# Optimization experiments

Measured on AMD Instinct MI355X. Metric: run time of the kernel, lower is better.

Reference implementation:

```python
import jax, jax.numpy as jnp
import numpy as np

POOL_H, POOL_W = 7, 7


def crop_and_resize(fmap, boxes, box_idx, ph, pw):
    """TF-style bilinear crop_and_resize. fmap [B,H,W,C], boxes [N,4] (y1,x1,y2,x2)
    normalized, box_idx [N] int32 -> [N,ph,pw,C]."""
    H, W = fmap.shape[1], fmap.shape[2]
    y1, x1, y2, x2 = boxes[:, 0], boxes[:, 1], boxes[:, 2], boxes[:, 3]
    gy = jnp.arange(ph, dtype=boxes.dtype) / (ph - 1)  # [ph]
    gx = jnp.arange(pw, dtype=boxes.dtype) / (pw - 1)  # [pw]
    in_y = (y1[:, None] + (y2 - y1)[:, None] * gy) * (H - 1)  # [N,ph]
    in_x = (x1[:, None] + (x2 - x1)[:, None] * gx) * (W - 1)  # [N,pw]
    y0f = jnp.floor(in_y)
    x0f = jnp.floor(in_x)
    wy = (in_y - y0f)[:, :, None, None]  # [N,ph,1,1]
    wx = (in_x - x0f)[:, None, :, None]  # [N,1,pw,1]
    y0 = jnp.clip(y0f.astype(jnp.int32), 0, H - 1)
    y1i = jnp.clip(y0 + 1, 0, H - 1)
    x0 = jnp.clip(x0f.astype(jnp.int32), 0, W - 1)
    x1i = jnp.clip(x0 + 1, 0, W - 1)
    b = box_idx[:, None, None]
    tl = fmap[b, y0[:, :, None], x0[:, None, :]]   # [N,ph,pw,C]
    tr = fmap[b, y0[:, :, None], x1i[:, None, :]]
    bl = fmap[b, y1i[:, :, None], x0[:, None, :]]
    br = fmap[b, y1i[:, :, None], x1i[:, None, :]]
    top = tl + (tr - tl) * wx
    bot = bl + (br - bl) * wx
    return top + (bot - top) * wy


def compute_roi_level(boxes, image_shape):
    # boxes [B,N,4] normalized (y1,x1,y2,x2)
    h = boxes[..., 2] - boxes[..., 0]
    w = boxes[..., 3] - boxes[..., 1]
    image_area = image_shape[0] * image_shape[1]
    lvl = jnp.log2(jnp.sqrt(h * w) / (224.0 / jnp.sqrt(image_area)))
    lvl = jnp.minimum(5.0, jnp.maximum(2.0, 4.0 + jnp.round(lvl)))
    return jax.lax.stop_gradient(lvl).astype(jnp.int32)  # [B,N]


def setup_inputs() -> dict:
    key = jax.random.key(0)
    kb, k2, k3, k4, k5 = jax.random.split(key, 5)
    B, N, C = 2, 1000, 256
    raw = jax.random.uniform(kb, (B, N, 2, 2), dtype=jnp.float32)
    lo = raw.min(axis=2)   # (y1, x1)
    hi = raw.max(axis=2)   # (y2, x2)
    boxes = jnp.concatenate([lo, hi], axis=-1)  # [B,N,4]
    image_shape = jnp.array([1024.0, 1024.0], dtype=jnp.float32)
    P2 = jax.random.normal(k2, (B, 256, 256, C), dtype=jnp.float32)
    P3 = jax.random.normal(k3, (B, 128, 128, C), dtype=jnp.float32)
    P4 = jax.random.normal(k4, (B, 64, 64, C), dtype=jnp.float32)
    P5 = jax.random.normal(k5, (B, 32, 32, C), dtype=jnp.float32)
    return {"boxes": boxes, "image_shape": image_shape,
            "P2": P2, "P3": P3, "P4": P4, "P5": P5}


def reference(boxes, image_shape, P2, P3, P4, P5):
    B, N = boxes.shape[0], boxes.shape[1]
    C = P2.shape[-1]
    levels = compute_roi_level(boxes, image_shape).reshape(-1)  # [B*N]
    flat_boxes = boxes.reshape(-1, 4)
    box_idx = jnp.repeat(jnp.arange(B, dtype=jnp.int32), N)
    pooled = jnp.zeros((B * N, POOL_H, POOL_W, C), dtype=P2.dtype)
    for lvl, fmap in zip((2, 3, 4, 5), (P2, P3, P4, P5)):
        crops = crop_and_resize(fmap, flat_boxes, box_idx, POOL_H, POOL_W)
        mask = (levels == lvl)[:, None, None, None]
        pooled = jnp.where(mask, crops, pooled)
    # The TF version partitions boxes per level then sorts back to original
    # (batch, box) order; the masked-select form yields the identical tensor.
    return pooled.reshape(B, N, POOL_H, POOL_W, C)
```

## Files before the change

### kernel.cpp

```cpp
#include <hip/hip_runtime.h>


#define POOL 7
#define CCH 256

__global__ __launch_bounds__(256) void roi_align_kernel(
    const float* __restrict__ boxes,
    const float* __restrict__ ish,
    const float* __restrict__ P2,
    const float* __restrict__ P3,
    const float* __restrict__ P4,
    const float* __restrict__ P5,
    float* __restrict__ out,
    int n_cells, int N)
{
    int cell = blockIdx.x * 4 + (threadIdx.x >> 6);
    if (cell >= n_cells) return;
    int lane = threadIdx.x & 63;

    int px  = cell % POOL;
    int t   = cell / POOL;
    int py  = t % POOL;
    int n   = t / POOL;
    int b   = n / N;

    float y1 = boxes[n * 4 + 0];
    float x1 = boxes[n * 4 + 1];
    float y2 = boxes[n * 4 + 2];
    float x2 = boxes[n * 4 + 3];
    float h = y2 - y1;
    float w = x2 - x1;

    float area = ish[0] * ish[1];
    float lvl  = log2f(sqrtf(h * w) / (224.0f / sqrtf(area)));
    float Lf   = fminf(5.0f, fmaxf(2.0f, 4.0f + rintf(lvl)));
    int   L    = (int)Lf;

    const float* fmap;
    int H;
    if (L == 2)      { fmap = P2; H = 256; }
    else if (L == 3) { fmap = P3; H = 128; }
    else if (L == 4) { fmap = P4; H = 64;  }
    else             { fmap = P5; H = 32;  }
    int W = H;

    float gy = (float)py / (float)(POOL - 1);
    float gx = (float)px / (float)(POOL - 1);
    float in_y = (y1 + h * gy) * (float)(H - 1);
    float in_x = (x1 + w * gx) * (float)(W - 1);
    float y0f = floorf(in_y);
    float x0f = floorf(in_x);
    float wy = in_y - y0f;
    float wx = in_x - x0f;
    int y0  = min(max((int)y0f, 0), H - 1);
    int y1i = min(y0 + 1, H - 1);
    int x0  = min(max((int)x0f, 0), W - 1);
    int x1i = min(x0 + 1, W - 1);

    size_t base = (size_t)b * H * W * CCH;
    const float* ptl = fmap + base + ((size_t)y0  * W + x0 ) * CCH;
    const float* ptr = fmap + base + ((size_t)y0  * W + x1i) * CCH;
    const float* pbl = fmap + base + ((size_t)y1i * W + x0 ) * CCH;
    const float* pbr = fmap + base + ((size_t)y1i * W + x1i) * CCH;

    int c = lane * 4;
    float4 tl = *(const float4*)(ptl + c);
    float4 tr = *(const float4*)(ptr + c);
    float4 bl = *(const float4*)(pbl + c);
    float4 br = *(const float4*)(pbr + c);

    float4 o;
    {
        float top, bot;
        top = tl.x + (tr.x - tl.x) * wx;
        bot = bl.x + (br.x - bl.x) * wx;
        o.x = top + (bot - top) * wy;
        top = tl.y + (tr.y - tl.y) * wx;
        bot = bl.y + (br.y - bl.y) * wx;
        o.y = top + (bot - top) * wy;
        top = tl.z + (tr.z - tl.z) * wx;
        bot = bl.z + (br.z - bl.z) * wx;
        o.z = top + (bot - top) * wy;
        top = tl.w + (tr.w - tl.w) * wx;
        bot = bl.w + (br.w - bl.w) * wx;
        o.w = top + (bot - top) * wy;
    }

    *(float4*)(out + (size_t)cell * CCH + c) = o;
}

extern "C" void kernel_launch(void* const* d_in, const int* in_sizes, int n_in,
                              void* d_out, int out_size, void* d_ws, size_t ws_size,
                              hipStream_t stream)
{
    const float* boxes = (const float*)d_in[0];
    const float* ish   = (const float*)d_in[1];
    const float* P2    = (const float*)d_in[2];
    const float* P3    = (const float*)d_in[3];
    const float* P4    = (const float*)d_in[4];
    const float* P5    = (const float*)d_in[5];
    float* out = (float*)d_out;

    int total_boxes = in_sizes[0] / 4;
    int B = in_sizes[2] / (256 * 256 * CCH);
    int N = total_boxes / B;
    int n_cells = total_boxes * POOL * POOL;

    int blocks = (n_cells + 3) / 4;
    roi_align_kernel<<<blocks, 256, 0, stream>>>(boxes, ish, P2, P3, P4, P5,
                                                 out, n_cells, N);
}
```

Before: 250.8 us.

## Process one pooled row per wavefront, reusing corner loads across columns

Each wavefront now handles a whole output row of seven cells instead of a single cell. It keeps the top/bottom corner vectors in registers and reuses them when consecutive columns share the same x0/x1 indices, so redundant gathers are skipped. Output writes use nontemporal stores, and the box and level computation is amortized across seven cells. In exchange there are fewer waves (seven times fewer blocks), which may reduce memory-level parallelism, and a serial dependency chain runs through the loop.

```diff
diff --git a/kernel.cpp b/kernel.cpp
--- a/kernel.cpp
+++ b/kernel.cpp
@@ -4,7 +4,9 @@
 #define POOL 7
 #define CCH 256
 
-__global__ __launch_bounds__(256) void roi_align_kernel(
+typedef float f4 __attribute__((ext_vector_type(4)));
+
+__global__ __launch_bounds__(256) void roi_align_row_kernel(
     const float* __restrict__ boxes,
     const float* __restrict__ ish,
     const float* __restrict__ P2,
@@ -12,17 +14,16 @@
     const float* __restrict__ P4,
     const float* __restrict__ P5,
     float* __restrict__ out,
-    int n_cells, int N)
+    int n_rows, int N)
 {
-    int cell = blockIdx.x * 4 + (threadIdx.x >> 6);
-    if (cell >= n_cells) return;
+    int row = blockIdx.x * 4 + (threadIdx.x >> 6);
+    if (row >= n_rows) return;
     int lane = threadIdx.x & 63;
+    int c = lane * 4;
 
-    int px  = cell % POOL;
-    int t   = cell / POOL;
-    int py  = t % POOL;
-    int n   = t / POOL;
-    int b   = n / N;
+    int py = row % POOL;
+    int n  = row / POOL;
+    int b  = n / N;
 
     float y1 = boxes[n * 4 + 0];
     float x1 = boxes[n * 4 + 1];
@@ -44,49 +45,54 @@
     else             { fmap = P5; H = 32;  }
     int W = H;
 
-    float gy = (float)py / (float)(POOL - 1);
-    float gx = (float)px / (float)(POOL - 1);
+    float gy   = (float)py * (1.0f / (POOL - 1));
     float in_y = (y1 + h * gy) * (float)(H - 1);
-    float in_x = (x1 + w * gx) * (float)(W - 1);
-    float y0f = floorf(in_y);
-    float x0f = floorf(in_x);
-    float wy = in_y - y0f;
-    float wx = in_x - x0f;
+    float y0f  = floorf(in_y);
+    float wy   = in_y - y0f;
     int y0  = min(max((int)y0f, 0), H - 1);
     int y1i = min(y0 + 1, H - 1);
-    int x0  = min(max((int)x0f, 0), W - 1);
-    int x1i = min(x0 + 1, W - 1);
 
-    size_t base = (size_t)b * H * W * CCH;
-    const float* ptl = fmap + base + ((size_t)y0  * W + x0 ) * CCH;
-    const float* ptr = fmap + base + ((size_t)y0  * W + x1i) * CCH;
-    const float* pbl = fmap + base + ((size_t)y1i * W + x0 ) * CCH;
-    const float* pbr = fmap + base + ((size_t)y1i * W + x1i) * CCH;
+    size_t base = (size_t)b * H * W * CCH + c;
+    const float* rt = fmap + base + (size_t)y0  * W * CCH;
+    const float* rb = fmap + base + (size_t)y1i * W * CCH;
 
-    int c = lane * 4;
-    float4 tl = *(const float4*)(ptl + c);
-    float4 tr = *(const float4*)(ptr + c);
-    float4 bl = *(const float4*)(pbl + c);
-    float4 br = *(const float4*)(pbr + c);
+    float* orow = out + ((size_t)n * (POOL * POOL) + (size_t)py * POOL) * CCH + c;
 
-    float4 o;
-    {
-        float top, bot;
-        top = tl.x + (tr.x - tl.x) * wx;
-        bot = bl.x + (br.x - bl.x) * wx;
-        o.x = top + (bot - top) * wy;
-        top = tl.y + (tr.y - tl.y) * wx;
-        bot = bl.y + (br.y - bl.y) * wx;
-        o.y = top + (bot - top) * wy;
-        top = tl.z + (tr.z - tl.z) * wx;
-        bot = bl.z + (br.z - bl.z) * wx;
-        o.z = top + (bot - top) * wy;
-        top = tl.w + (tr.w - tl.w) * wx;
-        bot = bl.w + (br.w - bl.w) * wx;
-        o.w = top + (bot - top) * wy;
+    int px0 = -100, px1 = -100;
+    f4 tl, tr, bl, br;
+
+    #pragma unroll
+    for (int px = 0; px < POOL; ++px) {
+        float gx   = (float)px * (1.0f / (POOL - 1));
+        float in_x = (x1 + w * gx) * (float)(W - 1);
+        float x0f  = floorf(in_x);
+        float wx   = in_x - x0f;
+        int x0  = min(max((int)x0f, 0), W - 1);
+        int x1i = min(x0 + 1, W - 1);
+
+        if (x0 == px0) {
+        } else if (x0 == px1) {
+            tl = tr; bl = br;
+            if (x1i != x0) {
+                tr = *(const f4*)(rt + (size_t)x1i * CCH);
+                br = *(const f4*)(rb + (size_t)x1i * CCH);
+            } else { tr = tl; br = bl; }
+        } else {
+            tl = *(const f4*)(rt + (size_t)x0 * CCH);
+            bl = *(const f4*)(rb + (size_t)x0 * CCH);
+            if (x1i != x0) {
+                tr = *(const f4*)(rt + (size_t)x1i * CCH);
+                br = *(const f4*)(rb + (size_t)x1i * CCH);
+            } else { tr = tl; br = bl; }
+        }
+        px0 = x0; px1 = x1i;
+
+        f4 top = tl + (tr - tl) * wx;
+        f4 bot = bl + (br - bl) * wx;
+        f4 o   = top + (bot - top) * wy;
+
+        __builtin_nontemporal_store(o, (f4*)(orow + (size_t)px * CCH));
     }
-
-    *(float4*)(out + (size_t)cell * CCH + c) = o;
 }
 
 extern "C" void kernel_launch(void* const* d_in, const int* in_sizes, int n_in,
@@ -104,9 +110,9 @@
     int total_boxes = in_sizes[0] / 4;
     int B = in_sizes[2] / (256 * 256 * CCH);
     int N = total_boxes / B;
-    int n_cells = total_boxes * POOL * POOL;
+    int n_rows = total_boxes * POOL;
 
-    int blocks = (n_cells + 3) / 4;
-    roi_align_kernel<<<blocks, 256, 0, stream>>>(boxes, ish, P2, P3, P4, P5,
-                                                 out, n_cells, N);
+    int blocks = (n_rows + 3) / 4;
+    roi_align_row_kernel<<<blocks, 256, 0, stream>>>(boxes, ish, P2, P3, P4, P5,
+                                                     out, n_rows, N);
 }
```

Result: no change. 253.1 us (+0.9%).
